# Kernel tuning notes

Measured on AMD Instinct MI355X. Metric: run time of the kernel, lower is better.

Reference implementation:

```python
import jax, jax.numpy as jnp
from jax import lax
import numpy as np

N, CH_I, CH_H, CH_Q, K, IMSIZE = 128, 2, 150, 10, 16, 64
EPS = 1e-5


def _conv(x, w):
    # 3x3, stride 1, pad 1 == SAME; NCHW / OIHW
    return lax.conv_general_dilated(x, w, (1, 1), 'SAME',
                                    dimension_numbers=('NCHW', 'OIHW', 'NCHW'))


def _maxpool2(x):
    return lax.reduce_window(x, -jnp.inf, lax.max, (1, 1, 2, 2), (1, 1, 2, 2), 'VALID')


def _upsample2(x):
    n, c, h, w = x.shape
    # torch Upsample(scale_factor=2, mode='bilinear', align_corners=False)
    return jax.image.resize(x, (n, c, 2 * h, 2 * w), method='linear')


def _vi_loop(new_r, conv_q_ws, denom):
    # value-iteration recurrence: rv = cat([new_r, v]); q = conv_i(rv); v = max_c q; sum += v
    v0 = jnp.zeros_like(new_r[:, :1])

    def step(carry, w):
        v, s = carry
        rv = jnp.concatenate([new_r, v], axis=1)
        q = _conv(rv, w)
        v = jnp.max(q, axis=1, keepdims=True)
        return (v, s + v), None

    (_, s), _ = lax.scan(step, (v0, v0), conv_q_ws)
    return s / denom


def setup_inputs() -> dict:
    key = jax.random.key(0)
    ks = jax.random.split(key, 12)
    g = lambda k, shp, fan: jax.random.normal(k, shp, dtype=jnp.float32) * (1.0 / np.sqrt(fan))
    X = jax.random.normal(ks[0], (N, CH_I, IMSIZE, IMSIZE), dtype=jnp.float32)
    S1 = jax.random.randint(ks[1], (N,), 0, IMSIZE)
    S2 = jax.random.randint(ks[2], (N,), 0, IMSIZE)
    return {
        'X': X, 'S1': S1, 'S2': S2,
        'conv_h_w': g(ks[3], (CH_H, CH_I, 3, 3), CH_I * 9),
        'conv_r_w': g(ks[4], (1, CH_H, 3, 3), CH_H * 9),
        'conv_q_ws': g(ks[5], (K, CH_Q, 3, 3, 3), 3 * 9),
        'bn_gamma': jnp.ones((CH_Q,), jnp.float32),
        'bn_beta': jnp.zeros((CH_Q,), jnp.float32),
        'duel_w1': g(ks[6], (1, CH_Q), CH_Q),
        'duel_w2': g(ks[7], (8, CH_Q), CH_Q),
        'vi_conv_h_w': g(ks[8], (150, 2, 3, 3), 2 * 9),
        'vi_conv_r_w': g(ks[9], (1, 150, 3, 3), 150 * 9),
        'vi_conv_q_ws': g(ks[10], (16, 10, 2, 3, 3), 2 * 9),
    }


def reference(X, S1, S2, conv_h_w, conv_r_w, conv_q_ws, bn_gamma, bn_beta,
              duel_w1, duel_w2, vi_conv_h_w, vi_conv_r_w, vi_conv_q_ws):
    # --- coarse branch (VImodel on pooled grid) ---
    X1 = _maxpool2(X)                               # [N,2,32,32]
    h1 = _conv(X1, vi_conv_h_w)                     # [N,150,32,32]
    r1 = _conv(h1, vi_conv_r_w)                     # [N,1,32,32]
    v1 = _vi_loop(r1, vi_conv_q_ws, 4.0)            # [N,1,32,32]
    m = _upsample2(v1)                              # [N,1,64,64]
    # --- fine branch ---
    h = _conv(X, conv_h_w)                          # [N,150,64,64]
    r = _conv(h, conv_r_w)                          # [N,1,64,64]
    new_r = jnp.concatenate([m, r], axis=1)         # [N,2,64,64]
    v = _vi_loop(new_r, conv_q_ws, float(K))        # [N,1,64,64]
    rv = jnp.concatenate([new_r, v], axis=1)        # [N,3,64,64]
    q = _conv(rv, conv_q_ws[K - 1])                 # [N,10,64,64]
    # BatchNorm2d (training-mode batch stats, biased variance)
    mean = jnp.mean(q, axis=(0, 2, 3), keepdims=True)
    var = jnp.var(q, axis=(0, 2, 3), keepdims=True)
    q = (q - mean) * jax.lax.rsqrt(var + EPS)
    q = q * bn_gamma[None, :, None, None] + bn_beta[None, :, None, None]
    # attention: q_out[n,c] = q[n, c, S1[n], S2[n]]
    q_out = q[jnp.arange(N), :, S1, S2]             # [N,10]
    # dueling head
    a = jax.nn.relu(q_out @ duel_w1.T)              # [N,1]
    b = jax.nn.relu(q_out @ duel_w2.T)              # [N,8]
    logits = a + (b - jnp.mean(b, axis=1, keepdims=True))
    return logits
```

## Files before the change

### kernel.cpp

```cpp
#include <hip/hip_runtime.h>


#define NEG_BIG (-3.402823466e38f)
#define SCOPE_AGENT __HIP_MEMORY_SCOPE_AGENT
#define WG_SCOPE    __HIP_MEMORY_SCOPE_WORKGROUP
#define CNT_BIG     0x3FFFFFFF

typedef __attribute__((ext_vector_type(8))) short bf16x8;
typedef __attribute__((ext_vector_type(4))) float f32x4;
typedef __attribute__((ext_vector_type(4))) unsigned int u32x4;

__device__ __forceinline__ unsigned f2bf(float f) {
    unsigned u = __builtin_bit_cast(unsigned, f);
    return (u + 0x7FFFu + ((u >> 16) & 1u)) >> 16;
}
__device__ __forceinline__ unsigned pk(float a, float b) {
    return f2bf(a) | (f2bf(b) << 16);
}

__global__ void k_precomp(const float* __restrict__ conv_h_w,
                          const float* __restrict__ conv_r_w,
                          const float* __restrict__ vi_h_w,
                          const float* __restrict__ vi_r_w,
                          const float* __restrict__ conv_q_ws,
                          float* __restrict__ ws) {
    __shared__ float sG[2][162];
    int t = threadIdx.x;
    if (t < 324) {
        int set = t / 162;
        int e   = t % 162;
        int ax = e % 3;  int e1 = e / 3;
        int ay = e1 % 3; int e2 = e1 / 3;
        int i  = e2 % 2; int e3 = e2 / 2;
        int bx = e3 % 3; int by = e3 / 3;
        const float* Wh = set ? vi_h_w : conv_h_w;
        const float* Wr = set ? vi_r_w : conv_r_w;
        float acc = 0.f;
        for (int c = 0; c < 150; ++c)
            acc += Wr[(c*3+by)*3+bx] * Wh[((c*2+i)*3+ay)*3+ax];
        sG[set][e] = acc;
        ws[(set ? 320 : 64) + e] = acc;
    }
    if (t >= 480 && t < 512) ws[512 + (t - 480)] = 0.f;
    for (int i = t; i < 8192; i += 1024) ((int*)ws)[4096 + i] = 0;
    {
        int s = t >> 6, lane = t & 63;
        int ch = lane & 15, kb = (lane >> 4) * 8;
        unsigned* dst = (unsigned*)(ws + 98304) + t * 4;
        for (int j = 0; j < 4; ++j) {
            int k0 = kb + 2*j, k1 = k0 + 1;
            float w0 = 0.f, w1 = 0.f;
            if (ch < 10) {
                if (k0 < 27) w0 = conv_q_ws[s*270 + ch*27 + (k0/9)*9 + (k0%9)];
                if (k1 < 27) w1 = conv_q_ws[s*270 + ch*27 + (k1/9)*9 + (k1%9)];
            }
            dst[j] = f2bf(w0) | (f2bf(w1) << 16);
        }
    }
    __syncthreads();
    if (t < 100) {
        int set = t / 50;
        int e   = t % 50;
        int i  = e / 25;
        int oy = (e % 25) / 5;
        int ox = e % 5;
        float acc = 0.f;
        for (int by = 0; by < 3; ++by) {
            int ay = oy - by; if (ay < 0 || ay > 2) continue;
            for (int bx = 0; bx < 3; ++bx) {
                int ax = ox - bx; if (ax < 0 || ax > 2) continue;
                acc += sG[set][(((by*3+bx)*2+i)*3+ay)*3+ax];
            }
        }
        ws[(set ? 256 : 0) + e] = acc;
    }
}

#define SPIN_NB(CNT, W, K)                                                    \
  { int sp_ = 0;                                                              \
    while (__hip_atomic_load(&CNT[(W)], __ATOMIC_ACQUIRE, WG_SCOPE) < (K) ||  \
           __hip_atomic_load(&CNT[(W)+2], __ATOMIC_ACQUIRE, WG_SCOPE) < (K)) {\
      if (++sp_ > (1 << 22)) break;                                           \
    } }

#define ISTEP(VC, VN, K)                                                      \
  {                                                                           \
    SPIN_NB(sCntI, rpw, (K));                                                 \
    const float* wk_ = vi_q_ws + (K) * 180;                                   \
    float pv_[3][3];                                                          \
    _Pragma("unroll") for (int dy = 0; dy < 3; ++dy)                          \
      _Pragma("unroll") for (int dx = 0; dx < 3; ++dx)                        \
        pv_[dy][dx] = VC[iy + dy][ix + dx];                                   \
    float m_ = NEG_BIG;                                                       \
    _Pragma("unroll") for (int ch = 0; ch < 10; ++ch) {                       \
      const float* wc_ = wk_ + ch * 18;                                       \
      float q_ = 0.f;                                                         \
      _Pragma("unroll") for (int ky = 0; ky < 3; ++ky)                        \
        _Pragma("unroll") for (int kx = 0; kx < 3; ++kx)                      \
          q_ += wc_[ky*3+kx] * prI[ky][kx] + wc_[9+ky*3+kx] * pv_[ky][kx];    \
      m_ = fmaxf(m_, q_);                                                     \
    }                                                                         \
    VN[1 + iy][1 + ix] = m_;                                                  \
    isum += m_;                                                               \
    if ((t & 63) == 0)                                                        \
      __hip_atomic_store(&sCntI[rpw + 1], (K) + 1, __ATOMIC_RELEASE, WG_SCOPE);\
  }

__global__
__attribute__((amdgpu_flat_work_group_size(1024, 1024), amdgpu_waves_per_eu(4, 4)))
void k_main(
    const float* __restrict__ Xg,
    const int*   __restrict__ S1,
    const int*   __restrict__ S2,
    const float* __restrict__ conv_q_ws,
    const float* __restrict__ vi_q_ws,
    const float* __restrict__ ws,
    float*       __restrict__ wsm)
{
    __shared__ float sX[2][64][64];
    __shared__ float sX1[2][32][32];
    __shared__ float sr1[34][34];
    __shared__ float sva[34][34];
    __shared__ float svb[34][34];
    __shared__ float sm[34][66];
    __shared__ float sr[34][66];
    __shared__ float sVb[34][66];
    __shared__ unsigned short vL[2][35][68];
    __shared__ unsigned int sA[16][64][4];
    __shared__ float sRed[10][2];
    __shared__ int sCntI[18];
    __shared__ int sCntO[18];

    const int bid  = blockIdx.x;
    const int half = (bid >> 3) & 1;
    const int n    = (bid & 7) | ((bid >> 4) << 3);
    const int gr0  = half << 5;
    const int t    = threadIdx.x;
    const int rpw  = t >> 6;

    int*   flagMine = (int*)wsm + 4096 + bid * 32;
    int*   flagPart = (int*)wsm + 4096 + (bid ^ 8) * 32;
    float* ghMine   = wsm + 16384 + bid * 256;
    float* ghPart   = wsm + 16384 + (bid ^ 8) * 256;

    {
        float* z;
        z = &sr1[0][0]; for (int i = t; i < 1156; i += 1024) z[i] = 0.f;
        z = &sva[0][0]; for (int i = t; i < 1156; i += 1024) z[i] = 0.f;
        z = &svb[0][0]; for (int i = t; i < 1156; i += 1024) z[i] = 0.f;
        z = &sm[0][0];  for (int i = t; i < 2244; i += 1024) z[i] = 0.f;
        z = &sr[0][0];  for (int i = t; i < 2244; i += 1024) z[i] = 0.f;
        z = &sVb[0][0]; for (int i = t; i < 2244; i += 1024) z[i] = 0.f;
        unsigned int* zv = (unsigned int*)&vL[0][0][0];
        for (int i = t; i < 2380; i += 1024) zv[i] = 0u;
        if (t < 20) ((float*)sRed)[t] = 0.f;
        if (t < 18) {
            sCntI[t] = (t == 0 || t == 17) ? CNT_BIG : 0;
            sCntO[t] = (t == 0 || t == 17) ? CNT_BIG : 0;
        }
        ((u32x4*)&sA[0][0][0])[t] = ((const u32x4*)(wsm + 98304))[t];
    }
    {
        const float4* src = (const float4*)(Xg + (size_t)n * 8192);
        float4* dst = (float4*)&sX[0][0][0];
        dst[t] = src[t];
        dst[t + 1024] = src[t + 1024];
    }
    __syncthreads();

    for (int idx = t; idx < 2048; idx += 1024) {
        int c = idx >> 10;
        int y = (idx >> 5) & 31;
        int x = idx & 31;
        float a0 = sX[c][2*y][2*x],   a1 = sX[c][2*y][2*x+1];
        float a2 = sX[c][2*y+1][2*x], a3 = sX[c][2*y+1][2*x+1];
        sX1[c][y][x] = fmaxf(fmaxf(a0, a1), fmaxf(a2, a3));
    }
    __syncthreads();

    const int iy = t >> 5, ix = t & 31;
    {
        const float* WeffI = ws + 256;
        const float* GI    = ws + 320;
        float acc = 0.f;
        for (int i = 0; i < 2; ++i)
            for (int oy = 0; oy < 5; ++oy) {
                int yy = iy + oy - 2; if (yy < 0 || yy >= 32) continue;
                for (int ox = 0; ox < 5; ++ox) {
                    int xx = ix + ox - 2; if (xx < 0 || xx >= 32) continue;
                    acc += WeffI[i*25 + oy*5 + ox] * sX1[i][yy][xx];
                }
            }
        if (iy == 0 || iy == 31 || ix == 0 || ix == 31) {
            float corr = 0.f;
            for (int by = 0; by < 3; ++by)
                for (int bx = 0; bx < 3; ++bx) {
                    int qy = iy + by - 1, qx = ix + bx - 1;
                    if (qy >= 0 && qy < 32 && qx >= 0 && qx < 32) continue;
                    const float* Gb = GI + (by*3+bx)*18;
                    for (int i = 0; i < 2; ++i)
                        for (int ay = 0; ay < 3; ++ay) {
                            int yy2 = qy + ay - 1; if (yy2 < 0 || yy2 >= 32) continue;
                            for (int ax = 0; ax < 3; ++ax) {
                                int xx2 = qx + ax - 1; if (xx2 < 0 || xx2 >= 32) continue;
                                corr += Gb[i*9 + ay*3 + ax] * sX1[i][yy2][xx2];
                            }
                        }
                }
            acc -= corr;
        }
        sr1[1+iy][1+ix] = acc;
    }
    __syncthreads();

    {
        float prI[3][3];
        #pragma unroll
        for (int dy = 0; dy < 3; ++dy)
            #pragma unroll
            for (int dx = 0; dx < 3; ++dx)
                prI[dy][dx] = sr1[iy+dy][ix+dx];
        float isum = 0.f;
        for (int k2 = 0; k2 < 8; ++k2) {
            ISTEP(sva, svb, 2*k2);
            ISTEP(svb, sva, 2*k2+1);
        }
        sr1[1+iy][1+ix] = isum * 0.25f;
    }
    __syncthreads();

    {
        const float* WeffO = ws;
        const float* GO    = ws + 64;
        int c = t & 63;
        for (int ar = t >> 6; ar < 34; ar += 16) {
            int g = gr0 + ar - 1;
            if ((unsigned)g < 64u) {
                int y0, y1; float wy0, wy1;
                if ((g & 1) == 0) { y1 = g >> 1; y0 = (y1 > 0) ? y1 - 1 : 0; wy1 = 0.75f; wy0 = 0.25f; }
                else              { y0 = g >> 1; y1 = (y0 < 31) ? y0 + 1 : 31; wy0 = 0.75f; wy1 = 0.25f; }
                int xa, xb; float wx0, wx1;
                if ((c & 1) == 0) { xb = c >> 1; xa = (xb > 0) ? xb - 1 : 0; wx1 = 0.75f; wx0 = 0.25f; }
                else              { xa = c >> 1; xb = (xa < 31) ? xa + 1 : 31; wx0 = 0.75f; wx1 = 0.25f; }
                sm[ar][1+c] = wy0 * (wx0 * sr1[1+y0][1+xa] + wx1 * sr1[1+y0][1+xb])
                            + wy1 * (wx0 * sr1[1+y1][1+xa] + wx1 * sr1[1+y1][1+xb]);
                float acc = 0.f;
                for (int i = 0; i < 2; ++i)
                    for (int oy = 0; oy < 5; ++oy) {
                        int yy = g + oy - 2; if (yy < 0 || yy >= 64) continue;
                        for (int ox = 0; ox < 5; ++ox) {
                            int xx = c + ox - 2; if (xx < 0 || xx >= 64) continue;
                            acc += WeffO[i*25 + oy*5 + ox] * sX[i][yy][xx];
                        }
                    }
                if (g == 0 || g == 63 || c == 0 || c == 63) {
                    float corr = 0.f;
                    for (int by = 0; by < 3; ++by)
                        for (int bx = 0; bx < 3; ++bx) {
                            int qy = g + by - 1, qx = c + bx - 1;
                            if (qy >= 0 && qy < 64 && qx >= 0 && qx < 64) continue;
                            const float* Gb = GO + (by*3+bx)*18;
                            for (int i = 0; i < 2; ++i)
                                for (int ay = 0; ay < 3; ++ay) {
                                    int yy2 = qy + ay - 1; if (yy2 < 0 || yy2 >= 64) continue;
                                    for (int ax = 0; ax < 3; ++ax) {
                                        int xx2 = qx + ax - 1; if (xx2 < 0 || xx2 >= 64) continue;
                                        corr += Gb[i*9 + ay*3 + ax] * sX[i][yy2][xx2];
                                    }
                                }
                        }
                    acc -= corr;
                }
                sr[ar][1+c] = acc;
            }
        }
    }
    __syncthreads();

    const int lane = t & 63;
    const int g    = lane >> 4;
    const int col  = lane & 15;
    const int rp   = rpw;
    const int pp   = half ? rp : (15 - rp);
    const int gRowV = half ? 0 : 33;

    unsigned Bs0[8], Bs1[8], Bs2[8], Bs3[8];
    #pragma unroll
    for (int tt = 0; tt < 8; ++tt) {
        const int lr = 2*pp + (tt >> 2);
        const int px = (tt & 3) * 16 + col;
        unsigned a0 = 0, a1 = 0, a2 = 0, a3 = 0;
        if (g == 0) {
            a0 = pk(sm[lr][px],     sm[lr][px+1]);
            a1 = pk(sm[lr][px+2],   sm[lr+1][px]);
            a2 = pk(sm[lr+1][px+1], sm[lr+1][px+2]);
            a3 = pk(sm[lr+2][px],   sm[lr+2][px+1]);
        } else if (g == 1) {
            a0 = pk(sm[lr+2][px+2], sr[lr][px]);
            a1 = pk(sr[lr][px+1],   sr[lr][px+2]);
            a2 = pk(sr[lr+1][px],   sr[lr+1][px+1]);
            a3 = pk(sr[lr+1][px+2], sr[lr+2][px]);
        } else if (g == 2) {
            a0 = pk(sr[lr+2][px+1], sr[lr+2][px+2]);
        }
        Bs0[tt] = a0; Bs1[tt] = a1; Bs2[tt] = a2; Bs3[tt] = a3;
    }

    float vsum[8];
    #pragma unroll
    for (int j = 0; j < 8; ++j) vsum[j] = 0.f;

    unsigned short*       ghU = (unsigned short*)ghMine;
    const unsigned short* gpU = (const unsigned short*)ghPart;

    for (int K = 0; K < 16; ++K) {
        const int cur = K & 1, nxt = cur ^ 1;
        union { u32x4 u; bf16x8 b; } av;
        av.u = *(const u32x4*)&sA[K][lane][0];
        SPIN_NB(sCntO, rp, K);
        #pragma unroll
        for (int tt = 0; tt < 8; ++tt) {
            const int lr = 2*pp + (tt >> 2);
            const int px = (tt & 3) * 16 + col;
            unsigned t01 = 0, t23 = 0, t45 = 0, v2 = 0;
            if (g >= 2) {
                const unsigned short* vp = &vL[cur][(g == 3) ? (lr + 2) : lr][px];
                unsigned v0 = vp[0], v1 = vp[1]; v2 = vp[2];
                unsigned v3 = vp[68], v4 = vp[69], v5 = vp[70];
                t01 = v0 | (v1 << 16);
                t23 = v2 | (v3 << 16);
                t45 = v4 | (v5 << 16);
            }
            union { u32x4 u; bf16x8 b; } bv;
            bv.u = (u32x4){
                (g == 3) ? t01 : Bs0[tt],
                (g == 2) ? t01 : ((g == 3) ? v2 : Bs1[tt]),
                (g == 2) ? t23 : Bs2[tt],
                (g == 2) ? t45 : Bs3[tt]};
            f32x4 d = __builtin_amdgcn_mfma_f32_16x16x32_bf16(
                av.b, bv.b, (f32x4){0.f, 0.f, 0.f, 0.f}, 0, 0, 0);
            float pm01 = fmaxf(d[0], d[1]);
            float pm4  = fmaxf(pm01, fmaxf(d[2], d[3]));
            float val  = (g < 2) ? pm4 : ((g == 2) ? pm01 : NEG_BIG);
            val = fmaxf(val, __shfl_xor(val, 16));
            val = fmaxf(val, __shfl_xor(val, 32));
            vsum[tt] += val;
            unsigned short vb = (unsigned short)f2bf(val);
            if (lane < 16) vL[nxt][lr + 1][px + 1] = vb;
            const bool btile = half ? (tt < 4) : (tt >= 4);
            if (K < 15 && rp == 0 && btile && lane < 16)
                ghU[cur * 64 + px] = vb;
        }
        if ((t & 63) == 0)
            __hip_atomic_store(&sCntO[rp + 1], K + 1, __ATOMIC_RELEASE, WG_SCOPE);
        if (K < 15 && rp == 0) {
            if (t == 0) {
                __hip_atomic_store(flagMine, K + 1, __ATOMIC_RELEASE, SCOPE_AGENT);
                int spins = 0;
                while (__hip_atomic_load(flagPart, __ATOMIC_ACQUIRE, SCOPE_AGENT) < K + 1)
                    if (++spins > (1 << 27)) break;
            }
            vL[nxt][gRowV][lane + 1] = gpU[cur * 64 + lane];
        }
    }
    __syncthreads();

    #pragma unroll
    for (int tt = 0; tt < 8; ++tt) {
        const int lr = 2*pp + (tt >> 2);
        const int px = (tt & 3) * 16 + col;
        if (lane < 16) sVb[lr + 1][px + 1] = vsum[tt];
    }
    if (rp == 0) {
        const int bAr = half ? 1 : 32;
        const int gAr = half ? 0 : 33;
        float sv = sVb[bAr][1 + lane];
        __hip_atomic_store(ghMine + 128 + lane, sv, __ATOMIC_RELAXED, SCOPE_AGENT);
        if (t == 0) {
            __hip_atomic_store(flagMine, 16, __ATOMIC_RELEASE, SCOPE_AGENT);
            int spins = 0;
            while (__hip_atomic_load(flagPart, __ATOMIC_ACQUIRE, SCOPE_AGENT) < 16)
                if (++spins > (1 << 27)) break;
        }
        sVb[gAr][1 + lane] =
            __hip_atomic_load(ghPart + 128 + lane, __ATOMIC_RELAXED, SCOPE_AGENT);
    }
    __syncthreads();

    {
        const float* wk = conv_q_ws + 15 * 270;
        const int oc = lane;
        float pm[4][3], pq[4][3], pv[4][3];
        #pragma unroll
        for (int dy = 0; dy < 4; ++dy)
            #pragma unroll
            for (int dx = 0; dx < 3; ++dx) {
                pm[dy][dx] = sm[2*pp+dy][oc+dx];
                pq[dy][dx] = sr[2*pp+dy][oc+dx];
                pv[dy][dx] = sVb[2*pp+dy][oc+dx] * 0.0625f;
            }
        int sy = S1[n], sx = S2[n];
        int ry0 = gr0 + 2*pp, ry1 = ry0 + 1;
        float* qpix = wsm + 544 + n * 10;
        #pragma unroll
        for (int ch = 0; ch < 10; ++ch) {
            const float* wc = wk + ch * 27;
            float q0 = 0.f, q1 = 0.f;
            #pragma unroll
            for (int ky = 0; ky < 3; ++ky)
                #pragma unroll
                for (int kx = 0; kx < 3; ++kx) {
                    float wm = wc[ky*3+kx];
                    float wr = wc[9  + ky*3+kx];
                    float wv = wc[18 + ky*3+kx];
                    q0 += wm * pm[ky][kx]   + wr * pq[ky][kx]   + wv * pv[ky][kx];
                    q1 += wm * pm[ky+1][kx] + wr * pq[ky+1][kx] + wv * pv[ky+1][kx];
                }
            if (oc == sx) {
                if (ry0 == sy) qpix[ch] = q0;
                if (ry1 == sy) qpix[ch] = q1;
            }
            float ls = q0 + q1, lq = q0*q0 + q1*q1;
            #pragma unroll
            for (int off = 32; off > 0; off >>= 1) {
                ls += __shfl_down(ls, off);
                lq += __shfl_down(lq, off);
            }
            if ((t & 63) == 0) {
                atomicAdd(&sRed[ch][0], ls);
                atomicAdd(&sRed[ch][1], lq);
            }
        }
        __syncthreads();
        if (t < 10) {
            atomicAdd(wsm + 512 + t, sRed[t][0]);
            atomicAdd(wsm + 528 + t, sRed[t][1]);
        }
    }
}

__global__ void k_final(const float* __restrict__ ws,
                        const float* __restrict__ gamma,
                        const float* __restrict__ beta,
                        const float* __restrict__ w1,
                        const float* __restrict__ w2,
                        float* __restrict__ out) {
    int n = threadIdx.x;
    if (n >= 128) return;
    const float inv = 1.f / 524288.f;
    float qn[10];
    for (int c = 0; c < 10; ++c) {
        float mean = ws[512 + c] * inv;
        float var  = ws[528 + c] * inv - mean * mean;
        float q    = ws[544 + n * 10 + c];
        qn[c] = (q - mean) * rsqrtf(var + 1e-5f) * gamma[c] + beta[c];
    }
    float a = 0.f;
    for (int c = 0; c < 10; ++c) a += qn[c] * w1[c];
    a = fmaxf(a, 0.f);
    float b[8], mb = 0.f;
    for (int j = 0; j < 8; ++j) {
        float bj = 0.f;
        for (int c = 0; c < 10; ++c) bj += qn[c] * w2[j * 10 + c];
        bj = fmaxf(bj, 0.f);
        b[j] = bj;
        mb += bj;
    }
    mb *= 0.125f;
    for (int j = 0; j < 8; ++j) out[n * 8 + j] = a + b[j] - mb;
}

extern "C" void kernel_launch(void* const* d_in, const int* in_sizes, int n_in,
                              void* d_out, int out_size, void* d_ws, size_t ws_size,
                              hipStream_t stream) {
    const float* X         = (const float*)d_in[0];
    const int*   S1        = (const int*)  d_in[1];
    const int*   S2        = (const int*)  d_in[2];
    const float* conv_h_w  = (const float*)d_in[3];
    const float* conv_r_w  = (const float*)d_in[4];
    const float* conv_q_ws = (const float*)d_in[5];
    const float* bn_gamma  = (const float*)d_in[6];
    const float* bn_beta   = (const float*)d_in[7];
    const float* duel_w1   = (const float*)d_in[8];
    const float* duel_w2   = (const float*)d_in[9];
    const float* vi_h_w    = (const float*)d_in[10];
    const float* vi_r_w    = (const float*)d_in[11];
    const float* vi_q_ws   = (const float*)d_in[12];
    float* ws = (float*)d_ws;

    k_precomp<<<1, 1024, 0, stream>>>(conv_h_w, conv_r_w, vi_h_w, vi_r_w,
                                      conv_q_ws, ws);
    k_main<<<256, 1024, 0, stream>>>(X, S1, S2, conv_q_ws, vi_q_ws, ws, ws);
    k_final<<<1, 128, 0, stream>>>(ws, bn_gamma, bn_beta, duel_w1, duel_w2,
                                   (float*)d_out);
}
```

Before: 187.8 us.

## Move coarse VI loop to bf16 MFMA and publish boundary rows earlier

The 32x32 coarse value-iteration loop used per-thread scalar FMAs (10 channels × 18 taps). It now runs on bf16 MFMA tiles with packed weights staged in shared memory and bf16 ping-pong value buffers. The fine loop processes the boundary-row tiles first, so the cross-block flag is released halfway through each step rather than at its end, shortening the partner's wait. The waves_per_eu attribute is removed, and the coarse path loses precision by moving from fp32 to bf16.

```diff
diff --git a/kernel.cpp b/kernel.cpp
--- a/kernel.cpp
+++ b/kernel.cpp
@@ -23,6 +23,7 @@
                           const float* __restrict__ vi_h_w,
                           const float* __restrict__ vi_r_w,
                           const float* __restrict__ conv_q_ws,
+                          const float* __restrict__ vi_q_ws,
                           float* __restrict__ ws) {
     __shared__ float sG[2][162];
     int t = threadIdx.x;
@@ -46,13 +47,27 @@
     {
         int s = t >> 6, lane = t & 63;
         int ch = lane & 15, kb = (lane >> 4) * 8;
-        unsigned* dst = (unsigned*)(ws + 98304) + t * 4;
+        unsigned* dst = (unsigned*)(ws + 81920) + t * 4;
         for (int j = 0; j < 4; ++j) {
             int k0 = kb + 2*j, k1 = k0 + 1;
             float w0 = 0.f, w1 = 0.f;
             if (ch < 10) {
-                if (k0 < 27) w0 = conv_q_ws[s*270 + ch*27 + (k0/9)*9 + (k0%9)];
-                if (k1 < 27) w1 = conv_q_ws[s*270 + ch*27 + (k1/9)*9 + (k1%9)];
+                if (k0 < 27) w0 = conv_q_ws[s*270 + ch*27 + k0];
+                if (k1 < 27) w1 = conv_q_ws[s*270 + ch*27 + k1];
+            }
+            dst[j] = f2bf(w0) | (f2bf(w1) << 16);
+        }
+    }
+    {
+        int s = t >> 6, lane = t & 63;
+        int ch = lane & 15, kb = (lane >> 4) * 8;
+        unsigned* dst = (unsigned*)(ws + 86016) + t * 4;
+        for (int j = 0; j < 4; ++j) {
+            int k0 = kb + 2*j, k1 = k0 + 1;
+            float w0 = 0.f, w1 = 0.f;
+            if (ch < 10) {
+                if (k0 < 18) w0 = vi_q_ws[s*180 + ch*18 + k0];
+                if (k1 < 18) w1 = vi_q_ws[s*180 + ch*18 + k1];
             }
             dst[j] = f2bf(w0) | (f2bf(w1) << 16);
         }
@@ -83,31 +98,43 @@
       if (++sp_ > (1 << 22)) break;                                           \
     } }
 
-#define ISTEP(VC, VN, K)                                                      \
+#define OTILE(TT)                                                             \
   {                                                                           \
-    SPIN_NB(sCntI, rpw, (K));                                                 \
-    const float* wk_ = vi_q_ws + (K) * 180;                                   \
-    float pv_[3][3];                                                          \
-    _Pragma("unroll") for (int dy = 0; dy < 3; ++dy)                          \
-      _Pragma("unroll") for (int dx = 0; dx < 3; ++dx)                        \
-        pv_[dy][dx] = VC[iy + dy][ix + dx];                                   \
-    float m_ = NEG_BIG;                                                       \
-    _Pragma("unroll") for (int ch = 0; ch < 10; ++ch) {                       \
-      const float* wc_ = wk_ + ch * 18;                                       \
-      float q_ = 0.f;                                                         \
-      _Pragma("unroll") for (int ky = 0; ky < 3; ++ky)                        \
-        _Pragma("unroll") for (int kx = 0; kx < 3; ++kx)                      \
-          q_ += wc_[ky*3+kx] * prI[ky][kx] + wc_[9+ky*3+kx] * pv_[ky][kx];    \
-      m_ = fmaxf(m_, q_);                                                     \
+    const int tt_ = (TT);                                                     \
+    const int lr  = 2*pp + (tt_ >> 2);                                        \
+    const int px  = (tt_ & 3) * 16 + col;                                     \
+    unsigned t01 = 0, t23 = 0, t45 = 0, v2 = 0;                               \
+    if (g >= 2) {                                                             \
+        const unsigned short* vp = &vL[cur][(g == 3) ? (lr + 2) : lr][px];    \
+        unsigned v0 = vp[0], v1 = vp[1]; v2 = vp[2];                          \
+        unsigned v3 = vp[68], v4 = vp[69], v5 = vp[70];                       \
+        t01 = v0 | (v1 << 16);                                                \
+        t23 = v2 | (v3 << 16);                                                \
+        t45 = v4 | (v5 << 16);                                                \
     }                                                                         \
-    VN[1 + iy][1 + ix] = m_;                                                  \
-    isum += m_;                                                               \
-    if ((t & 63) == 0)                                                        \
-      __hip_atomic_store(&sCntI[rpw + 1], (K) + 1, __ATOMIC_RELEASE, WG_SCOPE);\
+    union { u32x4 u; bf16x8 b; } bv;                                          \
+    bv.u = (u32x4){                                                           \
+        (g == 3) ? t01 : Bs0[tt_],                                            \
+        (g == 2) ? t01 : ((g == 3) ? v2 : Bs1[tt_]),                          \
+        (g == 2) ? t23 : Bs2[tt_],                                            \
+        (g == 2) ? t45 : Bs3[tt_]};                                           \
+    f32x4 d = __builtin_amdgcn_mfma_f32_16x16x32_bf16(                        \
+        av.b, bv.b, (f32x4){0.f, 0.f, 0.f, 0.f}, 0, 0, 0);                    \
+    float pm01 = fmaxf(d[0], d[1]);                                           \
+    float pm4  = fmaxf(pm01, fmaxf(d[2], d[3]));                              \
+    float val  = (g < 2) ? pm4 : ((g == 2) ? pm01 : NEG_BIG);                 \
+    val = fmaxf(val, __shfl_xor(val, 16));                                    \
+    val = fmaxf(val, __shfl_xor(val, 32));                                    \
+    vsum[tt_] += val;                                                         \
+    unsigned short vb = (unsigned short)f2bf(val);                            \
+    if (lane < 16) vL[nxt][lr + 1][px + 1] = vb;                              \
+    const bool btile = half ? (tt_ < 4) : (tt_ >= 4);                         \
+    if (K < 15 && rp == 0 && btile && lane < 16)                              \
+        ghU[cur * 64 + px] = vb;                 \
   }
 
 __global__
-__attribute__((amdgpu_flat_work_group_size(1024, 1024), amdgpu_waves_per_eu(4, 4)))
+__attribute__((amdgpu_flat_work_group_size(1024, 1024)))
 void k_main(
     const float* __restrict__ Xg,
     const int*   __restrict__ S1,
@@ -120,13 +147,13 @@
     __shared__ float sX[2][64][64];
     __shared__ float sX1[2][32][32];
     __shared__ float sr1[34][34];
-    __shared__ float sva[34][34];
-    __shared__ float svb[34][34];
     __shared__ float sm[34][66];
     __shared__ float sr[34][66];
     __shared__ float sVb[34][66];
     __shared__ unsigned short vL[2][35][68];
-    __shared__ unsigned int sA[16][64][4];
+    __shared__ unsigned short vI[2][34][36];
+    __shared__ unsigned int sA [16][64][4];
+    __shared__ unsigned int sAI[16][64][4];
     __shared__ float sRed[10][2];
     __shared__ int sCntI[18];
     __shared__ int sCntO[18];
@@ -137,6 +164,9 @@
     const int gr0  = half << 5;
     const int t    = threadIdx.x;
     const int rpw  = t >> 6;
+    const int lane = t & 63;
+    const int g    = lane >> 4;
+    const int col  = lane & 15;
 
     int*   flagMine = (int*)wsm + 4096 + bid * 32;
     int*   flagPart = (int*)wsm + 4096 + (bid ^ 8) * 32;
@@ -146,19 +176,20 @@
     {
         float* z;
         z = &sr1[0][0]; for (int i = t; i < 1156; i += 1024) z[i] = 0.f;
-        z = &sva[0][0]; for (int i = t; i < 1156; i += 1024) z[i] = 0.f;
-        z = &svb[0][0]; for (int i = t; i < 1156; i += 1024) z[i] = 0.f;
         z = &sm[0][0];  for (int i = t; i < 2244; i += 1024) z[i] = 0.f;
         z = &sr[0][0];  for (int i = t; i < 2244; i += 1024) z[i] = 0.f;
         z = &sVb[0][0]; for (int i = t; i < 2244; i += 1024) z[i] = 0.f;
         unsigned int* zv = (unsigned int*)&vL[0][0][0];
         for (int i = t; i < 2380; i += 1024) zv[i] = 0u;
+        unsigned int* zi = (unsigned int*)&vI[0][0][0];
+        for (int i = t; i < 1224; i += 1024) zi[i] = 0u;
         if (t < 20) ((float*)sRed)[t] = 0.f;
         if (t < 18) {
             sCntI[t] = (t == 0 || t == 17) ? CNT_BIG : 0;
             sCntO[t] = (t == 0 || t == 17) ? CNT_BIG : 0;
         }
-        ((u32x4*)&sA[0][0][0])[t] = ((const u32x4*)(wsm + 98304))[t];
+        ((u32x4*)&sA [0][0][0])[t] = ((const u32x4*)(wsm + 81920))[t];
+        ((u32x4*)&sAI[0][0][0])[t] = ((const u32x4*)(wsm + 86016))[t];
     }
     {
         const float4* src = (const float4*)(Xg + (size_t)n * 8192);
@@ -214,18 +245,72 @@
     __syncthreads();
 
     {
-        float prI[3][3];
+        unsigned BsI0[4], BsI1[4], BsI2[4], BsI3[4];
         #pragma unroll
-        for (int dy = 0; dy < 3; ++dy)
+        for (int tt = 0; tt < 4; ++tt) {
+            const int lr = 2*rpw + (tt >> 1);
+            const int px = (tt & 1) * 16 + col;
+            unsigned a0 = 0, a1 = 0, a2 = 0, a3 = 0;
+            if (g == 0) {
+                a0 = pk(sr1[lr][px],     sr1[lr][px+1]);
+                a1 = pk(sr1[lr][px+2],   sr1[lr+1][px]);
+                a2 = pk(sr1[lr+1][px+1], sr1[lr+1][px+2]);
+                a3 = pk(sr1[lr+2][px],   sr1[lr+2][px+1]);
+            } else if (g == 1) {
+                a0 = f2bf(sr1[lr+2][px+2]);
+            }
+            BsI0[tt] = a0; BsI1[tt] = a1; BsI2[tt] = a2; BsI3[tt] = a3;
+        }
+        float vsumI[4] = {0.f, 0.f, 0.f, 0.f};
+        for (int K = 0; K < 16; ++K) {
+            const int cur = K & 1, nxt = cur ^ 1;
+            union { u32x4 u; bf16x8 b; } av;
+            av.u = *(const u32x4*)&sAI[K][lane][0];
+            SPIN_NB(sCntI, rpw, K);
             #pragma unroll
-            for (int dx = 0; dx < 3; ++dx)
-                prI[dy][dx] = sr1[iy+dy][ix+dx];
-        float isum = 0.f;
-        for (int k2 = 0; k2 < 8; ++k2) {
-            ISTEP(sva, svb, 2*k2);
-            ISTEP(svb, sva, 2*k2+1);
-        }
-        sr1[1+iy][1+ix] = isum * 0.25f;
+            for (int tt = 0; tt < 4; ++tt) {
+                const int lr = 2*rpw + (tt >> 1);
+                const int px = (tt & 1) * 16 + col;
+                unsigned d0, d1, d2, d3;
+                if (g == 1) {
+                    const unsigned short* vp = &vI[cur][lr][px];
+                    unsigned w0 = vp[0], w1 = vp[1], w2v = vp[2];
+                    unsigned w3 = vp[36], w4 = vp[37], w5 = vp[38];
+                    unsigned w6 = vp[72];
+                    d0 = BsI0[tt] | (w0 << 16);
+                    d1 = w1 | (w2v << 16);
+                    d2 = w3 | (w4 << 16);
+                    d3 = w5 | (w6 << 16);
+                } else if (g == 2) {
+                    const unsigned short* vp = &vI[cur][lr+2][px+1];
+                    d0 = (unsigned)vp[0] | (((unsigned)vp[1]) << 16);
+                    d1 = 0; d2 = 0; d3 = 0;
+                } else if (g == 0) {
+                    d0 = BsI0[tt]; d1 = BsI1[tt]; d2 = BsI2[tt]; d3 = BsI3[tt];
+                } else {
+                    d0 = 0; d1 = 0; d2 = 0; d3 = 0;
+                }
+                union { u32x4 u; bf16x8 b; } bv;
+                bv.u = (u32x4){d0, d1, d2, d3};
+                f32x4 d = __builtin_amdgcn_mfma_f32_16x16x32_bf16(
+                    av.b, bv.b, (f32x4){0.f, 0.f, 0.f, 0.f}, 0, 0, 0);
+                float pm01 = fmaxf(d[0], d[1]);
+                float pm4  = fmaxf(pm01, fmaxf(d[2], d[3]));
+                float val  = (g < 2) ? pm4 : ((g == 2) ? pm01 : NEG_BIG);
+                val = fmaxf(val, __shfl_xor(val, 16));
+                val = fmaxf(val, __shfl_xor(val, 32));
+                vsumI[tt] += val;
+                if (lane < 16) vI[nxt][lr + 1][px + 1] = (unsigned short)f2bf(val);
+            }
+            if ((t & 63) == 0)
+                __hip_atomic_store(&sCntI[rpw + 1], K + 1, __ATOMIC_RELEASE, WG_SCOPE);
+        }
+        #pragma unroll
+        for (int tt = 0; tt < 4; ++tt) {
+            const int lr = 2*rpw + (tt >> 1);
+            const int px = (tt & 1) * 16 + col;
+            if (lane < 16) sr1[lr + 1][px + 1] = vsumI[tt] * 0.25f;
+        }
     }
     __syncthreads();
 
@@ -234,11 +319,11 @@
         const float* GO    = ws + 64;
         int c = t & 63;
         for (int ar = t >> 6; ar < 34; ar += 16) {
-            int g = gr0 + ar - 1;
-            if ((unsigned)g < 64u) {
+            int gg = gr0 + ar - 1;
+            if ((unsigned)gg < 64u) {
                 int y0, y1; float wy0, wy1;
-                if ((g & 1) == 0) { y1 = g >> 1; y0 = (y1 > 0) ? y1 - 1 : 0; wy1 = 0.75f; wy0 = 0.25f; }
-                else              { y0 = g >> 1; y1 = (y0 < 31) ? y0 + 1 : 31; wy0 = 0.75f; wy1 = 0.25f; }
+                if ((gg & 1) == 0) { y1 = gg >> 1; y0 = (y1 > 0) ? y1 - 1 : 0; wy1 = 0.75f; wy0 = 0.25f; }
+                else               { y0 = gg >> 1; y1 = (y0 < 31) ? y0 + 1 : 31; wy0 = 0.75f; wy1 = 0.25f; }
                 int xa, xb; float wx0, wx1;
                 if ((c & 1) == 0) { xb = c >> 1; xa = (xb > 0) ? xb - 1 : 0; wx1 = 0.75f; wx0 = 0.25f; }
                 else              { xa = c >> 1; xb = (xa < 31) ? xa + 1 : 31; wx0 = 0.75f; wx1 = 0.25f; }
@@ -247,17 +332,17 @@
                 float acc = 0.f;
                 for (int i = 0; i < 2; ++i)
                     for (int oy = 0; oy < 5; ++oy) {
-                        int yy = g + oy - 2; if (yy < 0 || yy >= 64) continue;
+                        int yy = gg + oy - 2; if (yy < 0 || yy >= 64) continue;
                         for (int ox = 0; ox < 5; ++ox) {
                             int xx = c + ox - 2; if (xx < 0 || xx >= 64) continue;
                             acc += WeffO[i*25 + oy*5 + ox] * sX[i][yy][xx];
                         }
                     }
-                if (g == 0 || g == 63 || c == 0 || c == 63) {
+                if (gg == 0 || gg == 63 || c == 0 || c == 63) {
                     float corr = 0.f;
                     for (int by = 0; by < 3; ++by)
                         for (int bx = 0; bx < 3; ++bx) {
-                            int qy = g + by - 1, qx = c + bx - 1;
+                            int qy = gg + by - 1, qx = c + bx - 1;
                             if (qy >= 0 && qy < 64 && qx >= 0 && qx < 64) continue;
                             const float* Gb = GO + (by*3+bx)*18;
                             for (int i = 0; i < 2; ++i)
@@ -277,9 +362,6 @@
     }
     __syncthreads();
 
-    const int lane = t & 63;
-    const int g    = lane >> 4;
-    const int col  = lane & 15;
     const int rp   = rpw;
     const int pp   = half ? rp : (15 - rp);
     const int gRowV = half ? 0 : 33;
@@ -318,44 +400,17 @@
         union { u32x4 u; bf16x8 b; } av;
         av.u = *(const u32x4*)&sA[K][lane][0];
         SPIN_NB(sCntO, rp, K);
+        const int swap = (rp == 0 && !half) ? 4 : 0;
         #pragma unroll
-        for (int tt = 0; tt < 8; ++tt) {
-            const int lr = 2*pp + (tt >> 2);
-            const int px = (tt & 3) * 16 + col;
-            unsigned t01 = 0, t23 = 0, t45 = 0, v2 = 0;
-            if (g >= 2) {
-                const unsigned short* vp = &vL[cur][(g == 3) ? (lr + 2) : lr][px];
-                unsigned v0 = vp[0], v1 = vp[1]; v2 = vp[2];
-                unsigned v3 = vp[68], v4 = vp[69], v5 = vp[70];
-                t01 = v0 | (v1 << 16);
-                t23 = v2 | (v3 << 16);
-                t45 = v4 | (v5 << 16);
-            }
-            union { u32x4 u; bf16x8 b; } bv;
-            bv.u = (u32x4){
-                (g == 3) ? t01 : Bs0[tt],
-                (g == 2) ? t01 : ((g == 3) ? v2 : Bs1[tt]),
-                (g == 2) ? t23 : Bs2[tt],
-                (g == 2) ? t45 : Bs3[tt]};
-            f32x4 d = __builtin_amdgcn_mfma_f32_16x16x32_bf16(
-                av.b, bv.b, (f32x4){0.f, 0.f, 0.f, 0.f}, 0, 0, 0);
-            float pm01 = fmaxf(d[0], d[1]);
-            float pm4  = fmaxf(pm01, fmaxf(d[2], d[3]));
-            float val  = (g < 2) ? pm4 : ((g == 2) ? pm01 : NEG_BIG);
-            val = fmaxf(val, __shfl_xor(val, 16));
-            val = fmaxf(val, __shfl_xor(val, 32));
-            vsum[tt] += val;
-            unsigned short vb = (unsigned short)f2bf(val);
-            if (lane < 16) vL[nxt][lr + 1][px + 1] = vb;
-            const bool btile = half ? (tt < 4) : (tt >= 4);
-            if (K < 15 && rp == 0 && btile && lane < 16)
-                ghU[cur * 64 + px] = vb;
-        }
+        for (int q8 = 0; q8 < 4; ++q8) OTILE(q8 ^ swap);
+        if (K < 15 && rp == 0 && t == 0)
+            __hip_atomic_store(flagMine, K + 1, __ATOMIC_RELEASE, SCOPE_AGENT);
+        #pragma unroll
+        for (int q8 = 4; q8 < 8; ++q8) OTILE(q8 ^ swap);
         if ((t & 63) == 0)
             __hip_atomic_store(&sCntO[rp + 1], K + 1, __ATOMIC_RELEASE, WG_SCOPE);
         if (K < 15 && rp == 0) {
             if (t == 0) {
-                __hip_atomic_store(flagMine, K + 1, __ATOMIC_RELEASE, SCOPE_AGENT);
                 int spins = 0;
                 while (__hip_atomic_load(flagPart, __ATOMIC_ACQUIRE, SCOPE_AGENT) < K + 1)
                     if (++spins > (1 << 27)) break;
@@ -489,7 +544,7 @@
     float* ws = (float*)d_ws;
 
     k_precomp<<<1, 1024, 0, stream>>>(conv_h_w, conv_r_w, vi_h_w, vi_r_w,
-                                      conv_q_ws, ws);
+                                      conv_q_ws, vi_q_ws, ws);
     k_main<<<256, 1024, 0, stream>>>(X, S1, S2, conv_q_ws, vi_q_ws, ws, ws);
     k_final<<<1, 128, 0, stream>>>(ws, bn_gamma, bn_beta, duel_w1, duel_w2,
                                    (float*)d_out);
```

New measurement: 171.6 us. 8.6% less time.
